# Kernel tuning notes

Measured on AMD Instinct MI355X. Metric: run time of the kernel, lower is better.

Reference implementation:

```python
import jax, jax.numpy as jnp
import numpy as np

B, T, D, H, L, F, V, BANDS = 16, 512, 1024, 8, 6, 4096, 30000, 16
RES = [1, 1, 2, 2, 4, 4, 8, 8]  # per-head K/V resolution schedule
HD = D // H


def setup_inputs() -> dict:
    key = jax.random.key(0)
    ks = iter(jax.random.split(key, 64))
    s = 0.02
    p = {
        "tokens": jax.random.randint(next(ks), (B, T), 0, V, dtype=jnp.int32),
        "embed": jax.random.normal(next(ks), (V, D), jnp.float32) * s,
        "pos_embed": jax.random.normal(next(ks), (T, D), jnp.float32) * s,
        "Wq": jax.random.normal(next(ks), (L, D, D), jnp.float32) * s,
        "bq": jnp.zeros((L, D), jnp.float32),
        "Wk": jax.random.normal(next(ks), (L, D, D), jnp.float32) * s,
        "bk": jnp.zeros((L, D), jnp.float32),
        "Wv": jax.random.normal(next(ks), (L, D, D), jnp.float32) * s,
        "bv": jnp.zeros((L, D), jnp.float32),
        "Wo": jax.random.normal(next(ks), (L, D, D), jnp.float32) * s,
        "bo": jnp.zeros((L, D), jnp.float32),
        "ln1_g": jnp.ones((L, D), jnp.float32),
        "ln1_b": jnp.zeros((L, D), jnp.float32),
        "ln2_g": jnp.ones((L, D), jnp.float32),
        "ln2_b": jnp.zeros((L, D), jnp.float32),
        "W1": jax.random.normal(next(ks), (L, D, F), jnp.float32) * s,
        "b1": jnp.zeros((L, F), jnp.float32),
        "W2": jax.random.normal(next(ks), (L, F, D), jnp.float32) * s,
        "b2": jnp.zeros((L, D), jnp.float32),
        "gates": jnp.ones((L, H, BANDS), jnp.float32),
        "lnf_g": jnp.ones((D,), jnp.float32),
        "lnf_b": jnp.zeros((D,), jnp.float32),
    }
    return p


def _ln(x, g, b, eps=1e-5):
    mu = jnp.mean(x, -1, keepdims=True)
    var = jnp.var(x, -1, keepdims=True)
    return (x - mu) * jax.lax.rsqrt(var + eps) * g + b


def _hfa_attention(x, Wq, bq, Wk, bk, Wv, bv, Wo, bo, gates_l):
    # x: [B,T,D]; per-head resolution schedule + spectral band gating.
    q = (x @ Wq + bq).reshape(B, T, H, HD).transpose(0, 2, 1, 3)  # [B,H,T,HD]
    k = (x @ Wk + bk).reshape(B, T, H, HD).transpose(0, 2, 1, 3)
    v = (x @ Wv + bv).reshape(B, T, H, HD).transpose(0, 2, 1, 3)
    nb = T // 2 + 1
    band_of_bin = (jnp.arange(nb) * BANDS) // nb  # map rfft bin -> spectral band
    scale = 1.0 / np.sqrt(HD)
    outs = []
    for h in range(H):
        r = RES[h]
        kh = k[:, h].reshape(B, T // r, r, HD).mean(2)  # pooled keys [B,T/r,HD]
        vh = v[:, h].reshape(B, T // r, r, HD).mean(2)
        scores = jnp.einsum("btd,bsd->bts", q[:, h], kh) * scale
        attn = jax.nn.softmax(scores, axis=-1)
        o = jnp.einsum("bts,bsd->btd", attn, vh)  # [B,T,HD]
        # spectral band gating along sequence axis
        g = gates_l[h][band_of_bin]  # [nb]
        f = jnp.fft.rfft(o, axis=1) * g[None, :, None]
        o = jnp.fft.irfft(f, n=T, axis=1)
        outs.append(o)
    out = jnp.concatenate(outs, axis=-1)  # [B,T,D]
    return out @ Wo + bo


def reference(tokens, embed, pos_embed, Wq, bq, Wk, bk, Wv, bv, Wo, bo,
              ln1_g, ln1_b, ln2_g, ln2_b, W1, b1, W2, b2, gates, lnf_g, lnf_b):
    x = embed[tokens] + pos_embed[jnp.arange(T)][None, :, :]  # [B,T,D]
    for l in range(L):
        h = _ln(x, ln1_g[l], ln1_b[l])
        x = x + _hfa_attention(h, Wq[l], bq[l], Wk[l], bk[l], Wv[l], bv[l],
                               Wo[l], bo[l], gates[l])
        h = _ln(x, ln2_g[l], ln2_b[l])
        ff = jax.nn.gelu(h @ W1[l] + b1[l], approximate=False) @ W2[l] + b2[l]
        x = x + ff
    return _ln(x, lnf_g, lnf_b)
```

## Files before the change

kernel.cpp:

```cpp
#include <hip/hip_runtime.h>
#include <hip/hip_bf16.h>
#include <math.h>

#define Bn 16
#define Tn 512
#define Dn 1024
#define Hn 8
#define Ln 6
#define Fn 4096
#define HDn 128

typedef __attribute__((ext_vector_type(8))) short short8;
typedef __attribute__((ext_vector_type(4))) float f32x4;

__device__ __forceinline__ float bf2f(unsigned short u){
  union{float f; unsigned int i;} c; c.i = ((unsigned int)u)<<16; return c.f;
}
__device__ __forceinline__ unsigned short f2bf(float f){
  union{float f; unsigned int i;} c; c.f=f;
  unsigned int r = c.i + 0x7fffu + ((c.i>>16)&1u);
  return (unsigned short)(r>>16);
}
__device__ __forceinline__ int pref_of(int h){
  int g = h >> 1;
  return (2048 - (2048 >> g)) + (h & 1) * (512 >> g);
}

#define GLOAD(gp, lp) __builtin_amdgcn_global_load_lds( \
    (const __attribute__((address_space(1))) void*)(const void*)(gp), \
    (__attribute__((address_space(3))) void*)(void*)(lp), 16, 0, 0)

__global__ __launch_bounds__(256) void embed_kernel(
    const int* __restrict__ tok, const float* __restrict__ emb,
    const float* __restrict__ pos, float* __restrict__ x){
  long row = blockIdx.x;
  int t = (int)(row & (Tn-1));
  int tk = tok[row];
  int d = threadIdx.x*4;
  float4 e = *(const float4*)(emb + (long)tk*Dn + d);
  float4 p = *(const float4*)(pos + (long)t*Dn + d);
  float4 r; r.x=e.x+p.x; r.y=e.y+p.y; r.z=e.z+p.z; r.w=e.w+p.w;
  *(float4*)(x + row*(long)Dn + d) = r;
}

template<int OUTBF>
__global__ __launch_bounds__(256) void ln_kernel(
    const float* __restrict__ x, const float* __restrict__ g,
    const float* __restrict__ b, void* __restrict__ outp){
  long row = blockIdx.x;
  const float* xr = x + row*(long)Dn;
  int tid = threadIdx.x;
  float4 v4 = *(const float4*)(xr + tid*4);
  float s  = v4.x+v4.y+v4.z+v4.w;
  float s2 = v4.x*v4.x + v4.y*v4.y + v4.z*v4.z + v4.w*v4.w;
  #pragma unroll
  for (int o=32;o;o>>=1){ s += __shfl_xor(s,o); s2 += __shfl_xor(s2,o); }
  __shared__ float rs[4], rs2[4];
  int w = tid>>6;
  if ((tid&63)==0){ rs[w]=s; rs2[w]=s2; }
  __syncthreads();
  s  = rs[0]+rs[1]+rs[2]+rs[3];
  s2 = rs2[0]+rs2[1]+rs2[2]+rs2[3];
  float mu  = s*(1.f/Dn);
  float var = s2*(1.f/Dn) - mu*mu;
  float rstd = rsqrtf(var + 1e-5f);
  float4 gg = *(const float4*)(g + tid*4);
  float4 bb = *(const float4*)(b + tid*4);
  float o0 = (v4.x-mu)*rstd*gg.x + bb.x;
  float o1 = (v4.y-mu)*rstd*gg.y + bb.y;
  float o2 = (v4.z-mu)*rstd*gg.z + bb.z;
  float o3 = (v4.w-mu)*rstd*gg.w + bb.w;
  if (OUTBF){
    unsigned short* o = (unsigned short*)outp + row*(long)Dn + tid*4;
    o[0]=f2bf(o0); o[1]=f2bf(o1); o[2]=f2bf(o2); o[3]=f2bf(o3);
  } else {
    float* o = (float*)outp + row*(long)Dn + tid*4;
    o[0]=o0; o[1]=o1; o[2]=o2; o[3]=o3;
  }
}

__global__ __launch_bounds__(256) void transpose_w(
    const float* __restrict__ W, unsigned short* __restrict__ WT, int Kd, int Nd){
  __shared__ float tile[32][33];
  long lofs = (long)blockIdx.z * Kd * Nd;
  int n0 = blockIdx.x*32, k0 = blockIdx.y*32;
  int tx = threadIdx.x & 31, ty = threadIdx.x >> 5;
  #pragma unroll
  for (int i=0;i<4;i++){
    int kk = k0 + ty + i*8;
    tile[ty+i*8][tx] = W[lofs + (long)kk*Nd + n0 + tx];
  }
  __syncthreads();
  #pragma unroll
  for (int i=0;i<4;i++){
    int nn = n0 + ty + i*8;
    WT[lofs + (long)nn*Kd + k0 + tx] = f2bf(tile[tx][ty+i*8]);
  }
}

__global__ __launch_bounds__(256) void pack_bias(
    const float* __restrict__ bq, const float* __restrict__ bk,
    const float* __restrict__ bv, float* __restrict__ bqkv){
  int i = blockIdx.x*256 + threadIdx.x;
  int l = i / (3*Dn); int r = i - l*3*Dn; int w = r / Dn; int d = r - w*Dn;
  const float* src = (w==0)? bq : ((w==1)? bk : bv);
  bqkv[i] = src[l*Dn + d];
}

__global__ __launch_bounds__(512) void ckern(
    const float* __restrict__ gates, float* __restrict__ cbuf){
  int lh = blockIdx.x;
  __shared__ float gb[16];
  if (threadIdx.x < 16) gb[threadIdx.x] = gates[lh*16 + threadIdx.x];
  __syncthreads();
  int m = threadIdx.x;
  float acc = gb[0];
  for (int j=1;j<256;j++){
    int band = (j*16)/257;
    int kmod = (j*m) & 511;
    acc += 2.f*gb[band]*cosf(1.2271846303085129e-2f * (float)kmod);
  }
  acc += gb[15] * ((m & 1) ? -1.f : 1.f);
  cbuf[lh*512 + m] = acc * (1.f/512.f);
}

__global__ __launch_bounds__(256) void gfill(
    const float* __restrict__ cbuf, unsigned short* __restrict__ G){
  long idx = (long)blockIdx.x*256 + threadIdx.x;
  int lh = (int)(idx >> 18);
  int rem = (int)(idx & 262143);
  int t = rem >> 9, s = rem & 511;
  G[idx] = f2bf(cbuf[lh*512 + ((t - s) & 511)]);
}

__global__ __launch_bounds__(256) void pool_kernel(
    const unsigned short* __restrict__ kin, const unsigned short* __restrict__ vin,
    unsigned short* __restrict__ kp, unsigned short* __restrict__ vTp){
  long idx = (long)blockIdx.x*256 + threadIdx.x;
  if (idx >= (long)Bn*1920*HDn) return;
  long rem = idx; int hh = 0; int S = 512;
  for (hh=0; hh<8; hh++){
    S = 512 >> (hh>>1);
    long seg = (long)Bn*S*HDn;
    if (rem < seg) break;
    rem -= seg;
  }
  int r = 512 / S;
  int d = (int)(rem % HDn);
  long t2 = rem / HDn;
  int s = (int)(t2 % S);
  int b = (int)(t2 / S);
  const unsigned short* kb = kin + ((long)(b*Tn + s*r))*Dn + hh*HDn + d;
  const unsigned short* vb = vin + ((long)(b*Tn + s*r))*Dn + hh*HDn + d;
  float ks=0.f, vs=0.f;
  for (int j=0;j<r;j++){ ks += bf2f(kb[(long)j*Dn]); vs += bf2f(vb[(long)j*Dn]); }
  float inv = 1.f/(float)r;
  int pref=0;
  for (int g2=0; g2<hh; g2++) pref += 512 >> (g2>>1);
  long segb = (long)Bn*HDn*pref;
  kp [segb + ((long)b*S + s)*HDn + d] = f2bf(ks*inv);
  vTp[segb + ((long)b*HDn + d)*S + s] = f2bf(vs*inv);
}

__global__ __launch_bounds__(256) void softmax_all(
    const float* __restrict__ sc, unsigned short* __restrict__ at){
  long rid = (long)blockIdx.x*4 + (threadIdx.x >> 6);
  int head = (int)(rid >> 13);
  int rih  = (int)(rid & 8191);
  int g = head >> 1;
  int S = 512 >> g;
  int NV = S >> 6;
  long base = (long)Bn*Tn*pref_of(head) + (long)rih*S;
  const float* r = sc + base;
  int lane = threadIdx.x & 63;
  float vals[8];
  float mx = -1e30f;
  #pragma unroll
  for (int i=0;i<8;i++){
    if (i < NV){ vals[i] = r[lane + i*64] * 0.08838834764831845f; mx = fmaxf(mx, vals[i]); }
  }
  #pragma unroll
  for (int o=32;o;o>>=1) mx = fmaxf(mx, __shfl_xor(mx, o));
  float sum = 0.f;
  #pragma unroll
  for (int i=0;i<8;i++){
    if (i < NV){ vals[i] = expf(vals[i]-mx); sum += vals[i]; }
  }
  #pragma unroll
  for (int o=32;o;o>>=1) sum += __shfl_xor(sum, o);
  float inv = 1.f/sum;
  unsigned short* ab = at + base;
  #pragma unroll
  for (int i=0;i<8;i++){
    if (i < NV) ab[lane + i*64] = f2bf(vals[i]*inv);
  }
}

template<int MODE>
__global__ __launch_bounds__(256)
void gemm_kernel(const unsigned short* __restrict__ A, int lda, long sAb, long sAh,
                 const unsigned short* __restrict__ Bt, int ldb, long sBb, long sBh,
                 void* __restrict__ Cout, int ldc, long sCb, long sCh,
                 const float* __restrict__ bias, long sbias,
                 int zshift, int zmask,
                 int M, int N, int K)
{
  __shared__ unsigned short AB[2][2][128*64];
  int z = blockIdx.z;
  int zb = z & zmask, zh = z >> zshift;
  const unsigned short* Az = A + (long)zb*sAb + (long)zh*sAh;
  const unsigned short* Bz = Bt + (long)zb*sBb + (long)zh*sBh;
  const float* biasz = bias ? (bias + (long)zh*sbias) : nullptr;
  int m0 = blockIdx.y*128, n0 = blockIdx.x*128;
  int tid = threadIdx.x;
  int lane = tid & 63, wid = tid >> 6;
  int wm = wid >> 1, wn = wid & 1;
  f32x4 zero4 = {0.f,0.f,0.f,0.f};
  f32x4 acc[4][4];
  #pragma unroll
  for (int m=0;m<4;m++)
    #pragma unroll
    for (int n=0;n<4;n++)
      acc[m][n] = zero4;
  const int r16 = lane & 15, kq = lane >> 4;

  auto stage = [&](int buf, int k0){
    #pragma unroll
    for (int i=0;i<4;i++){
      int chunk = i*256 + tid;
      int row = chunk >> 3, c = chunk & 7;
      int cg = (c ^ (row & 7)) * 8;
      int gm = m0 + row; gm = gm < M ? gm : M-1;
      GLOAD(Az + (long)gm*lda + k0 + cg, AB[buf][0] + (i*256 + wid*64)*8);
    }
    #pragma unroll
    for (int i=0;i<4;i++){
      int chunk = i*256 + tid;
      int row = chunk >> 3, c = chunk & 7;
      int cg = (c ^ (row & 7)) * 8;
      int gn = n0 + row; gn = gn < N ? gn : N-1;
      GLOAD(Bz + (long)gn*ldb + k0 + cg, AB[buf][1] + (i*256 + wid*64)*8);
    }
  };

  int NT = K >> 6;
  stage(0, 0);
  for (int t = 0; t < NT; t++){
    if (t + 1 < NT){
      stage((t+1)&1, (t+1)*64);
      asm volatile("s_waitcnt vmcnt(8)" ::: "memory");
    } else {
      asm volatile("s_waitcnt vmcnt(0)" ::: "memory");
    }
    __builtin_amdgcn_s_barrier();
    const unsigned short* As = AB[t&1][0];
    const unsigned short* Bs = AB[t&1][1];
    #pragma unroll
    for (int kk=0; kk<64; kk+=32){
      short8 af[4], bfr[4];
      int kb = (kk + kq*8) * 2;
      #pragma unroll
      for (int m=0;m<4;m++){
        int row = wm*64 + m*16 + r16;
        af[m] = *(const short8*)((const char*)As + row*128 + (kb ^ ((row & 7) << 4)));
      }
      #pragma unroll
      for (int n=0;n<4;n++){
        int row = wn*64 + n*16 + r16;
        bfr[n] = *(const short8*)((const char*)Bs + row*128 + (kb ^ ((row & 7) << 4)));
      }
      #pragma unroll
      for (int m=0;m<4;m++)
        #pragma unroll
        for (int n=0;n<4;n++)
          acc[m][n] = __builtin_amdgcn_mfma_f32_16x16x32_bf16(af[m], bfr[n], acc[m][n], 0, 0, 0);
    }
    __builtin_amdgcn_s_barrier();
  }
  #pragma unroll
  for (int n=0;n<4;n++){
    int col = n0 + wn*64 + n*16 + r16;
    if (col >= N) continue;
    float bvv = 0.f;
    if (MODE != 0 && biasz != nullptr) bvv = biasz[col];
    #pragma unroll
    for (int m=0;m<4;m++){
      #pragma unroll
      for (int e=0;e<4;e++){
        int row = m0 + wm*64 + m*16 + kq*4 + e;
        if (row >= M) continue;
        float vv = acc[m][n][e] + bvv;
        long cidx = (long)zb*sCb + (long)zh*sCh + (long)row*ldc + col;
        if (MODE == 0)      ((float*)Cout)[cidx] = vv;
        else                ((unsigned short*)Cout)[cidx] = f2bf(vv);
      }
    }
  }
}

__global__ __launch_bounds__(256)
void scores_all(const unsigned short* __restrict__ q,
                const unsigned short* __restrict__ kp,
                float* __restrict__ sc)
{
  __shared__ unsigned short AB[2][2][128*64];
  int z = blockIdx.z;
  int zb = z & 15, zh = z >> 4;
  int g = zh >> 1;
  int S = 512 >> g;
  int n0 = blockIdx.x*128;
  if (n0 >= S) return;
  int pf = pref_of(zh);
  const unsigned short* Az = q  + (long)zb*Tn*Dn + (long)zh*HDn;
  const unsigned short* Bz = kp + (long)Bn*HDn*pf + (long)zb*S*HDn;
  float* Cz = sc + (long)Bn*Tn*pf + (long)zb*Tn*S;
  int m0 = blockIdx.y*128;
  int tid = threadIdx.x;
  int lane = tid & 63, wid = tid >> 6;
  int wm = wid >> 1, wn = wid & 1;
  f32x4 zero4 = {0.f,0.f,0.f,0.f};
  f32x4 acc[4][4];
  #pragma unroll
  for (int m=0;m<4;m++)
    #pragma unroll
    for (int n=0;n<4;n++)
      acc[m][n] = zero4;
  const int r16 = lane & 15, kq = lane >> 4;

  auto stage = [&](int buf, int k0){
    #pragma unroll
    for (int i=0;i<4;i++){
      int chunk = i*256 + tid;
      int row = chunk >> 3, c = chunk & 7;
      int cg = (c ^ (row & 7)) * 8;
      GLOAD(Az + (long)(m0 + row)*Dn + k0 + cg, AB[buf][0] + (i*256 + wid*64)*8);
    }
    #pragma unroll
    for (int i=0;i<4;i++){
      int chunk = i*256 + tid;
      int row = chunk >> 3, c = chunk & 7;
      int cg = (c ^ (row & 7)) * 8;
      int gn = n0 + row; gn = gn < S ? gn : S-1;
      GLOAD(Bz + (long)gn*HDn + k0 + cg, AB[buf][1] + (i*256 + wid*64)*8);
    }
  };

  stage(0, 0);
  stage(1, 64);
  #pragma unroll
  for (int t = 0; t < 2; t++){
    if (t == 0) { asm volatile("s_waitcnt vmcnt(8)" ::: "memory"); }
    else        { asm volatile("s_waitcnt vmcnt(0)" ::: "memory"); }
    __builtin_amdgcn_s_barrier();
    const unsigned short* As = AB[t][0];
    const unsigned short* Bs = AB[t][1];
    #pragma unroll
    for (int kk=0; kk<64; kk+=32){
      short8 af[4], bfr[4];
      int kb = (kk + kq*8) * 2;
      #pragma unroll
      for (int m=0;m<4;m++){
        int row = wm*64 + m*16 + r16;
        af[m] = *(const short8*)((const char*)As + row*128 + (kb ^ ((row & 7) << 4)));
      }
      #pragma unroll
      for (int n=0;n<4;n++){
        int row = wn*64 + n*16 + r16;
        bfr[n] = *(const short8*)((const char*)Bs + row*128 + (kb ^ ((row & 7) << 4)));
      }
      #pragma unroll
      for (int m=0;m<4;m++)
        #pragma unroll
        for (int n=0;n<4;n++)
          acc[m][n] = __builtin_amdgcn_mfma_f32_16x16x32_bf16(af[m], bfr[n], acc[m][n], 0, 0, 0);
    }
    __builtin_amdgcn_s_barrier();
  }
  #pragma unroll
  for (int n=0;n<4;n++){
    int col = n0 + wn*64 + n*16 + r16;
    if (col >= S) continue;
    #pragma unroll
    for (int m=0;m<4;m++){
      #pragma unroll
      for (int e=0;e<4;e++){
        int row = m0 + wm*64 + m*16 + kq*4 + e;
        Cz[(long)row*S + col] = acc[m][n][e];
      }
    }
  }
}

__global__ __launch_bounds__(256)
void pv_all(const unsigned short* __restrict__ vTp,
            const unsigned short* __restrict__ at,
            unsigned short* __restrict__ oT)
{
  __shared__ unsigned short AB[2][2][128*64];
  int z = blockIdx.z;
  int zb = z & 15, zh = z >> 4;
  int g = zh >> 1;
  int S = 512 >> g;
  int pf = pref_of(zh);
  const unsigned short* Az = vTp + (long)Bn*HDn*pf + (long)zb*HDn*S;
  const unsigned short* Bz = at  + (long)Bn*Tn*pf  + (long)zb*Tn*S;
  unsigned short* Cz = oT + (long)zh*Bn*HDn*Tn + (long)zb*HDn*Tn;
  int n0 = blockIdx.x*128;
  int tid = threadIdx.x;
  int lane = tid & 63, wid = tid >> 6;
  int wm = wid >> 1, wn = wid & 1;
  f32x4 zero4 = {0.f,0.f,0.f,0.f};
  f32x4 acc[4][4];
  #pragma unroll
  for (int m=0;m<4;m++)
    #pragma unroll
    for (int n=0;n<4;n++)
      acc[m][n] = zero4;
  const int r16 = lane & 15, kq = lane >> 4;

  auto stage = [&](int buf, int k0){
    #pragma unroll
    for (int i=0;i<4;i++){
      int chunk = i*256 + tid;
      int row = chunk >> 3, c = chunk & 7;
      int cg = (c ^ (row & 7)) * 8;
      GLOAD(Az + (long)row*S + k0 + cg, AB[buf][0] + (i*256 + wid*64)*8);
    }
    #pragma unroll
    for (int i=0;i<4;i++){
      int chunk = i*256 + tid;
      int row = chunk >> 3, c = chunk & 7;
      int cg = (c ^ (row & 7)) * 8;
      GLOAD(Bz + (long)(n0 + row)*S + k0 + cg, AB[buf][1] + (i*256 + wid*64)*8);
    }
  };

  int NT = S >> 6;
  stage(0, 0);
  for (int t = 0; t < NT; t++){
    if (t + 1 < NT){
      stage((t+1)&1, (t+1)*64);
      asm volatile("s_waitcnt vmcnt(8)" ::: "memory");
    } else {
      asm volatile("s_waitcnt vmcnt(0)" ::: "memory");
    }
    __builtin_amdgcn_s_barrier();
    const unsigned short* As = AB[t&1][0];
    const unsigned short* Bs = AB[t&1][1];
    #pragma unroll
    for (int kk=0; kk<64; kk+=32){
      short8 af[4], bfr[4];
      int kb = (kk + kq*8) * 2;
      #pragma unroll
      for (int m=0;m<4;m++){
        int row = wm*64 + m*16 + r16;
        af[m] = *(const short8*)((const char*)As + row*128 + (kb ^ ((row & 7) << 4)));
      }
      #pragma unroll
      for (int n=0;n<4;n++){
        int row = wn*64 + n*16 + r16;
        bfr[n] = *(const short8*)((const char*)Bs + row*128 + (kb ^ ((row & 7) << 4)));
      }
      #pragma unroll
      for (int m=0;m<4;m++)
        #pragma unroll
        for (int n=0;n<4;n++)
          acc[m][n] = __builtin_amdgcn_mfma_f32_16x16x32_bf16(af[m], bfr[n], acc[m][n], 0, 0, 0);
    }
    __builtin_amdgcn_s_barrier();
  }
  #pragma unroll
  for (int n=0;n<4;n++){
    int col = n0 + wn*64 + n*16 + r16;
    #pragma unroll
    for (int m=0;m<4;m++){
      #pragma unroll
      for (int e=0;e<4;e++){
        int row = wm*64 + m*16 + kq*4 + e;
        Cz[(long)row*Tn + col] = f2bf(acc[m][n][e]);
      }
    }
  }
}

template<int MODE, int Mt, int Nt, int Kt, long SBH, long SCH, int BIASST>
__global__ __launch_bounds__(256)
void gemm_big(const unsigned short* __restrict__ A,
              const unsigned short* __restrict__ Bt,
              void* __restrict__ Cout,
              const float* __restrict__ bias)
{
  __shared__ char shraw[2][32768];
  int zh = blockIdx.z;
  const unsigned short* Bz = Bt + (long)zh*SBH;
  const float* biasz = bias + (long)zh*BIASST;
  int m0 = blockIdx.y*128, n0 = blockIdx.x*128;
  int tid = threadIdx.x;
  int lane = tid & 63, wid = tid >> 6;
  int wm = wid >> 1, wn = wid & 1;
  f32x4 zero4 = {0.f,0.f,0.f,0.f};
  f32x4 acc[4][4];
  #pragma unroll
  for (int m=0;m<4;m++)
    #pragma unroll
    for (int n=0;n<4;n++)
      acc[m][n] = zero4;
  const int r16 = lane & 15, kq = lane >> 4;

  const unsigned short* pA[4];
  const unsigned short* pB[4];
  #pragma unroll
  for (int i=0;i<4;i++){
    int chunk = i*256 + tid;
    int row = chunk >> 3, c = chunk & 7;
    int cg = (c ^ (row & 7)) * 8;
    pA[i] = A  + (long)(m0 + row)*Kt + cg;
    pB[i] = Bz + (long)(n0 + row)*Kt + cg;
  }
  auto stage = [&](int buf, int k0){
    unsigned short* As = (unsigned short*)shraw[buf];
    #pragma unroll
    for (int i=0;i<4;i++) GLOAD(pA[i] + k0, As + (i*256 + wid*64)*8);
    #pragma unroll
    for (int i=0;i<4;i++) GLOAD(pB[i] + k0, As + 8192 + (i*256 + wid*64)*8);
  };

  constexpr int NT = Kt/64;
  stage(0, 0);
  for (int t = 0; t < NT; t++){
    if (t + 1 < NT){
      stage((t+1)&1, (t+1)*64);
      asm volatile("s_waitcnt vmcnt(8)" ::: "memory");
    } else {
      asm volatile("s_waitcnt vmcnt(0)" ::: "memory");
    }
    __builtin_amdgcn_s_barrier();
    const unsigned short* As = (const unsigned short*)shraw[t&1];
    const unsigned short* Bs = As + 8192;
    #pragma unroll
    for (int kk=0; kk<64; kk+=32){
      short8 af[4], bfr[4];
      int kb = (kk + kq*8) * 2;
      #pragma unroll
      for (int m=0;m<4;m++){
        int row = wm*64 + m*16 + r16;
        af[m] = *(const short8*)((const char*)As + row*128 + (kb ^ ((row & 7) << 4)));
      }
      #pragma unroll
      for (int n=0;n<4;n++){
        int row = wn*64 + n*16 + r16;
        bfr[n] = *(const short8*)((const char*)Bs + row*128 + (kb ^ ((row & 7) << 4)));
      }
      #pragma unroll
      for (int m=0;m<4;m++)
        #pragma unroll
        for (int n=0;n<4;n++)
          acc[m][n] = __builtin_amdgcn_mfma_f32_16x16x32_bf16(af[m], bfr[n], acc[m][n], 0, 0, 0);
    }
    __builtin_amdgcn_s_barrier();
  }

  if (MODE == 1 || MODE == 2){
    unsigned short* shb = (unsigned short*)&shraw[0][0];
    #pragma unroll
    for (int n=0;n<4;n++){
      int col = wn*64 + n*16 + r16;
      float bvv = biasz[n0 + col];
      #pragma unroll
      for (int m=0;m<4;m++){
        #pragma unroll
        for (int e=0;e<4;e++){
          int row = wm*64 + m*16 + kq*4 + e;
          float vv = acc[m][n][e] + bvv;
          if (MODE == 2) vv = 0.5f*vv*(1.f + erff(vv*0.7071067811865475f));
          shb[row*136 + col] = f2bf(vv);
        }
      }
    }
    __syncthreads();
    #pragma unroll
    for (int i=0;i<8;i++){
      int chunk = i*256 + tid;
      int row = chunk >> 4, col = (chunk & 15)*8;
      short8 vv8 = *(const short8*)(shb + row*136 + col);
      *(short8*)((unsigned short*)Cout + (long)zh*SCH +
                 (long)(m0 + row)*Nt + n0 + col) = vv8;
    }
  } else {
    float* shf = (float*)&shraw[0][0];
    #pragma unroll
    for (int ph=0; ph<2; ph++){
      __syncthreads();
      if (wm == ph){
        #pragma unroll
        for (int n=0;n<4;n++){
          int col = wn*64 + n*16 + r16;
          float bvv = biasz[n0 + col];
          #pragma unroll
          for (int m=0;m<4;m++){
            #pragma unroll
            for (int e=0;e<4;e++){
              int rl = m*16 + kq*4 + e;
              shf[rl*136 + col] = acc[m][n][e] + bvv;
            }
          }
        }
      }
      __syncthreads();
      #pragma unroll
      for (int i=0;i<8;i++){
        int chunk = i*256 + tid;
        int row = chunk >> 5, col = (chunk & 31)*4;
        float4 vv = *(const float4*)(shf + row*136 + col);
        float* cp = (float*)Cout + (long)(m0 + ph*64 + row)*Nt + n0 + col;
        float4 o = *(const float4*)cp;
        o.x += vv.x; o.y += vv.y; o.z += vv.z; o.w += vv.w;
        *(float4*)cp = o;
      }
    }
  }
}

extern "C" void kernel_launch(void* const* d_in, const int* in_sizes, int n_in,
                              void* d_out, int out_size, void* d_ws, size_t ws_size,
                              hipStream_t stream){
  const int*   tokens = (const int*)  d_in[0];
  const float* embedp = (const float*)d_in[1];
  const float* pos    = (const float*)d_in[2];
  const float* Wq  = (const float*)d_in[3];
  const float* bq  = (const float*)d_in[4];
  const float* Wk  = (const float*)d_in[5];
  const float* bk  = (const float*)d_in[6];
  const float* Wv  = (const float*)d_in[7];
  const float* bv  = (const float*)d_in[8];
  const float* Wo  = (const float*)d_in[9];
  const float* bo  = (const float*)d_in[10];
  const float* ln1g= (const float*)d_in[11];
  const float* ln1b= (const float*)d_in[12];
  const float* ln2g= (const float*)d_in[13];
  const float* ln2b= (const float*)d_in[14];
  const float* W1  = (const float*)d_in[15];
  const float* b1  = (const float*)d_in[16];
  const float* W2  = (const float*)d_in[17];
  const float* b2  = (const float*)d_in[18];
  const float* gates=(const float*)d_in[19];
  const float* lnfg= (const float*)d_in[20];
  const float* lnfb= (const float*)d_in[21];
  float* out = (float*)d_out;

  char* base = (char*)d_ws;
  size_t off = 0;
  auto take = [&](size_t bytes)->char*{
    char* p = base + off;
    off = (off + bytes + 255) & ~(size_t)255;
    return p;
  };
  unsigned short* WqT = (unsigned short*)take((size_t)Ln*Dn*Dn*2);
  unsigned short* WkT = (unsigned short*)take((size_t)Ln*Dn*Dn*2);
  unsigned short* WvT = (unsigned short*)take((size_t)Ln*Dn*Dn*2);
  unsigned short* WoT = (unsigned short*)take((size_t)Ln*Dn*Dn*2);
  unsigned short* W1T = (unsigned short*)take((size_t)Ln*Dn*Fn*2);
  unsigned short* W2T = (unsigned short*)take((size_t)Ln*Dn*Fn*2);
  unsigned short* G   = (unsigned short*)take((size_t)Ln*Hn*Tn*Tn*2);
  float*          cbuf= (float*)take((size_t)Ln*Hn*Tn*4);
  float*          bqkv= (float*)take((size_t)Ln*3*Dn*4);
  float*          x   = (float*)take((size_t)Bn*Tn*Dn*4);
  unsigned short* hbuf= (unsigned short*)take((size_t)Bn*Tn*Dn*2);
  unsigned short* q   = (unsigned short*)take((size_t)Bn*Tn*Dn*2);
  unsigned short* k   = (unsigned short*)take((size_t)Bn*Tn*Dn*2);
  unsigned short* v   = (unsigned short*)take((size_t)Bn*Tn*Dn*2);
  unsigned short* kp  = (unsigned short*)take((size_t)Bn*1920*HDn*2);
  unsigned short* vTp = (unsigned short*)take((size_t)Bn*1920*HDn*2);
  unsigned short* ao  = (unsigned short*)take((size_t)Bn*Tn*Dn*2);
  unsigned short* ff1 = (unsigned short*)take((size_t)Bn*Tn*Fn*2);
  unsigned short* attnA = (unsigned short*)take((size_t)Bn*1920*Tn*2);
  if (off > ws_size) return;
  float* scoresA = (float*)ff1;
  unsigned short* oT = k;

  transpose_w<<<dim3(Dn/32, Dn/32, Ln), 256, 0, stream>>>(Wq, WqT, Dn, Dn);
  transpose_w<<<dim3(Dn/32, Dn/32, Ln), 256, 0, stream>>>(Wk, WkT, Dn, Dn);
  transpose_w<<<dim3(Dn/32, Dn/32, Ln), 256, 0, stream>>>(Wv, WvT, Dn, Dn);
  transpose_w<<<dim3(Dn/32, Dn/32, Ln), 256, 0, stream>>>(Wo, WoT, Dn, Dn);
  transpose_w<<<dim3(Fn/32, Dn/32, Ln), 256, 0, stream>>>(W1, W1T, Dn, Fn);
  transpose_w<<<dim3(Dn/32, Fn/32, Ln), 256, 0, stream>>>(W2, W2T, Fn, Dn);
  pack_bias<<<(Ln*3*Dn)/256, 256, 0, stream>>>(bq, bk, bv, bqkv);
  ckern<<<Ln*Hn, 512, 0, stream>>>(gates, cbuf);
  gfill<<<(Ln*Hn*Tn*Tn)/256, 256, 0, stream>>>(cbuf, G);
  embed_kernel<<<Bn*Tn, 256, 0, stream>>>(tokens, embedp, pos, x);

  const int MT = Bn*Tn;

  for (int l=0; l<Ln; l++){
    ln_kernel<1><<<MT, 256, 0, stream>>>(x, ln1g + l*Dn, ln1b + l*Dn, hbuf);
    gemm_big<1, 8192, Dn, Dn, (long)Ln*Dn*Dn, (long)Bn*Tn*Dn, Dn>
        <<<dim3(Dn/128, MT/128, 3), 256, 0, stream>>>(
        hbuf, WqT + (size_t)l*Dn*Dn, q, bqkv + (size_t)l*3*Dn);
    pool_kernel<<<((long)Bn*1920*HDn + 255)/256, 256, 0, stream>>>(k, v, kp, vTp);

    scores_all<<<dim3(4, Tn/128, 128), 256, 0, stream>>>(q, kp, scoresA);
    softmax_all<<<(8*MT)/4, 256, 0, stream>>>(scoresA, attnA);
    pv_all<<<dim3(Tn/128, 1, 128), 256, 0, stream>>>(vTp, attnA, oT);

    gemm_kernel<1><<<dim3(1, Tn/128, 128), 256, 0, stream>>>(
        G + (size_t)(l*Hn)*Tn*Tn, Tn, 0L, (long)Tn*Tn,
        oT, Tn, (long)HDn*Tn, (long)Bn*HDn*Tn,
        ao, Dn, (long)Tn*Dn, (long)HDn,
        nullptr, 0L, 4, 15,
        Tn, HDn, Tn);
    gemm_big<3, 8192, Dn, Dn, 0L, 0L, 0>
        <<<dim3(Dn/128, MT/128, 1), 256, 0, stream>>>(
        ao, WoT + (size_t)l*Dn*Dn, x, bo + l*Dn);
    ln_kernel<1><<<MT, 256, 0, stream>>>(x, ln2g + l*Dn, ln2b + l*Dn, hbuf);
    gemm_big<2, 8192, Fn, Dn, 0L, 0L, 0>
        <<<dim3(Fn/128, MT/128, 1), 256, 0, stream>>>(
        hbuf, W1T + (size_t)l*Dn*Fn, ff1, b1 + l*Fn);
    gemm_big<3, 8192, Dn, Fn, 0L, 0L, 0>
        <<<dim3(Dn/128, MT/128, 1), 256, 0, stream>>>(
        ff1, W2T + (size_t)l*Dn*Fn, x, b2 + l*Dn);
  }
  ln_kernel<0><<<MT, 256, 0, stream>>>(x, lnfg, lnfb, out);
}
```

Before: 2.877 ms.

## Pool LN output before K/V projection to shrink K/V GEMM work

Pooling and linear projection commute, so the normalized activations are mean-pooled per resolution group first and the K/V projections run only on the pooled rows, grouped per head pair. Packed K/V weights and biases are built once at setup, and a small transpose kernel produces the V-transposed layout. This removes the full-resolution K and V GEMMs for the coarser heads and the separate pool pass over K/V. The main GEMM's pipeline is also reordered to wait after compute and to raise wave priority around the MFMA block, which may reduce load/compute overlap.

Measured after the change: 2.777 ms. -3.5%, faster.

```diff
diff --git a/kernel.cpp b/kernel.cpp
--- a/kernel.cpp
+++ b/kernel.cpp
@@ -11,6 +11,7 @@
 #define HDn 128
 
 typedef __attribute__((ext_vector_type(8))) short short8;
+typedef __attribute__((ext_vector_type(4))) short short4v;
 typedef __attribute__((ext_vector_type(4))) float f32x4;
 
 __device__ __forceinline__ float bf2f(unsigned short u){
@@ -24,6 +25,9 @@
 __device__ __forceinline__ int pref_of(int h){
   int g = h >> 1;
   return (2048 - (2048 >> g)) + (h & 1) * (512 >> g);
+}
+__device__ __forceinline__ int kvoff_of(int g){
+  return (g==0)?0:(g==1)?8192:(g==2)?12288:14336;
 }
 
 #define GLOAD(gp, lp) __builtin_amdgcn_global_load_lds( \
@@ -98,13 +102,28 @@
   }
 }
 
-__global__ __launch_bounds__(256) void pack_bias(
-    const float* __restrict__ bq, const float* __restrict__ bk,
-    const float* __restrict__ bv, float* __restrict__ bqkv){
+__global__ __launch_bounds__(256) void pack_wkv(
+    const unsigned short* __restrict__ WkT, const unsigned short* __restrict__ WvT,
+    unsigned short* __restrict__ wkvT){
+  int i8 = blockIdx.x*256 + threadIdx.x;
+  int c8 = i8 & 127;
+  int r  = (i8 >> 7) & 511;
+  int g  = (i8 >> 16) & 3;
+  int l  = i8 >> 18;
+  const unsigned short* src = (r < 256)
+      ? WkT + ((long)l<<20) + (long)(g*256 + r)*1024 + c8*8
+      : WvT + ((long)l<<20) + (long)(g*256 + (r-256))*1024 + c8*8;
+  *(short8*)(wkvT + (long)i8*8) = *(const short8*)src;
+}
+
+__global__ __launch_bounds__(256) void pack_bkv(
+    const float* __restrict__ bk, const float* __restrict__ bv,
+    float* __restrict__ bkv){
   int i = blockIdx.x*256 + threadIdx.x;
-  int l = i / (3*Dn); int r = i - l*3*Dn; int w = r / Dn; int d = r - w*Dn;
-  const float* src = (w==0)? bq : ((w==1)? bk : bv);
-  bqkv[i] = src[l*Dn + d];
+  int c = i & 511;
+  int g = (i >> 9) & 3;
+  int l = i >> 11;
+  bkv[i] = (c < 256) ? bk[l*1024 + g*256 + c] : bv[l*1024 + g*256 + (c-256)];
 }
 
 __global__ __launch_bounds__(512) void ckern(
@@ -133,33 +152,52 @@
   G[idx] = f2bf(cbuf[lh*512 + ((t - s) & 511)]);
 }
 
-__global__ __launch_bounds__(256) void pool_kernel(
-    const unsigned short* __restrict__ kin, const unsigned short* __restrict__ vin,
-    unsigned short* __restrict__ kp, unsigned short* __restrict__ vTp){
-  long idx = (long)blockIdx.x*256 + threadIdx.x;
-  if (idx >= (long)Bn*1920*HDn) return;
-  long rem = idx; int hh = 0; int S = 512;
-  for (hh=0; hh<8; hh++){
-    S = 512 >> (hh>>1);
-    long seg = (long)Bn*S*HDn;
-    if (rem < seg) break;
-    rem -= seg;
-  }
-  int r = 512 / S;
-  int d = (int)(rem % HDn);
-  long t2 = rem / HDn;
-  int s = (int)(t2 % S);
-  int b = (int)(t2 / S);
-  const unsigned short* kb = kin + ((long)(b*Tn + s*r))*Dn + hh*HDn + d;
-  const unsigned short* vb = vin + ((long)(b*Tn + s*r))*Dn + hh*HDn + d;
-  float ks=0.f, vs=0.f;
-  for (int j=0;j<r;j++){ ks += bf2f(kb[(long)j*Dn]); vs += bf2f(vb[(long)j*Dn]); }
+__global__ __launch_bounds__(256) void pool_x(
+    const unsigned short* __restrict__ hbuf, unsigned short* __restrict__ P){
+  int rid = blockIdx.x;
+  int g, S, idx;
+  if (rid < 4096){ g=1; S=256; idx=rid; }
+  else if (rid < 6144){ g=2; S=128; idx=rid-4096; }
+  else { g=3; S=64; idx=rid-6144; }
+  int r = 1 << g;
+  int b = idx / S, s = idx - b*S;
+  const unsigned short* src = hbuf + ((long)(b*512 + s*r))*1024 + threadIdx.x*4;
+  float a0=0.f, a1=0.f, a2=0.f, a3=0.f;
+  for (int j=0;j<r;j++){
+    short4v v = *(const short4v*)(src + (long)j*1024);
+    a0 += bf2f((unsigned short)v[0]); a1 += bf2f((unsigned short)v[1]);
+    a2 += bf2f((unsigned short)v[2]); a3 += bf2f((unsigned short)v[3]);
+  }
   float inv = 1.f/(float)r;
-  int pref=0;
-  for (int g2=0; g2<hh; g2++) pref += 512 >> (g2>>1);
-  long segb = (long)Bn*HDn*pref;
-  kp [segb + ((long)b*S + s)*HDn + d] = f2bf(ks*inv);
-  vTp[segb + ((long)b*HDn + d)*S + s] = f2bf(vs*inv);
+  unsigned short* dst = P + (long)rid*1024 + threadIdx.x*4;
+  dst[0]=f2bf(a0*inv); dst[1]=f2bf(a1*inv); dst[2]=f2bf(a2*inv); dst[3]=f2bf(a3*inv);
+}
+
+__global__ __launch_bounds__(256) void vtrans(
+    const unsigned short* __restrict__ kvbuf, unsigned short* __restrict__ vTp){
+  __shared__ unsigned short tile[32][33];
+  int z = blockIdx.z;
+  int h = z >> 4, b = z & 15;
+  int g = h >> 1, dlt = h & 1;
+  int S = 512 >> g;
+  int s0 = blockIdx.x*32;
+  if (s0 >= S) return;
+  int d0 = blockIdx.y*32;
+  int kvbase = kvoff_of(g) + b*S;
+  int colbase = 256 + dlt*128 + d0;
+  int tx = threadIdx.x & 31, ty = threadIdx.x >> 5;
+  #pragma unroll
+  for (int i=0;i<4;i++){
+    int s = s0 + ty + i*8;
+    tile[ty+i*8][tx] = kvbuf[(long)(kvbase + s)*512 + colbase + tx];
+  }
+  __syncthreads();
+  long basep = (long)Bn*HDn*pref_of(h);
+  #pragma unroll
+  for (int i=0;i<4;i++){
+    int d = d0 + ty + i*8;
+    vTp[basep + ((long)(b*128 + d))*S + s0 + tx] = tile[tx][ty+i*8];
+  }
 }
 
 __global__ __launch_bounds__(256) void softmax_all(
@@ -300,19 +338,19 @@
 
 __global__ __launch_bounds__(256)
 void scores_all(const unsigned short* __restrict__ q,
-                const unsigned short* __restrict__ kp,
+                const unsigned short* __restrict__ kvbuf,
                 float* __restrict__ sc)
 {
   __shared__ unsigned short AB[2][2][128*64];
   int z = blockIdx.z;
   int zb = z & 15, zh = z >> 4;
-  int g = zh >> 1;
+  int g = zh >> 1, dlt = zh & 1;
   int S = 512 >> g;
   int n0 = blockIdx.x*128;
   if (n0 >= S) return;
   int pf = pref_of(zh);
-  const unsigned short* Az = q  + (long)zb*Tn*Dn + (long)zh*HDn;
-  const unsigned short* Bz = kp + (long)Bn*HDn*pf + (long)zb*S*HDn;
+  const unsigned short* Az = q + (long)zb*Tn*Dn + (long)zh*HDn;
+  const unsigned short* Bz = kvbuf + (long)(kvoff_of(g) + zb*S)*512 + dlt*128;
   float* Cz = sc + (long)Bn*Tn*pf + (long)zb*Tn*S;
   int m0 = blockIdx.y*128;
   int tid = threadIdx.x;
@@ -341,7 +379,7 @@
       int row = chunk >> 3, c = chunk & 7;
       int cg = (c ^ (row & 7)) * 8;
       int gn = n0 + row; gn = gn < S ? gn : S-1;
-      GLOAD(Bz + (long)gn*HDn + k0 + cg, AB[buf][1] + (i*256 + wid*64)*8);
+      GLOAD(Bz + (long)gn*512 + k0 + cg, AB[buf][1] + (i*256 + wid*64)*8);
     }
   };
 
@@ -483,6 +521,112 @@
   }
 }
 
+__global__ __launch_bounds__(256)
+void gemm_kv(const unsigned short* __restrict__ hbuf,
+             const unsigned short* __restrict__ P,
+             const unsigned short* __restrict__ wkvT_l,
+             unsigned short* __restrict__ kvbuf,
+             const float* __restrict__ bkv_l)
+{
+  __shared__ char shraw[2][32768];
+  int zh = blockIdx.z;
+  int Mg = 8192 >> zh;
+  int m0 = blockIdx.y*128;
+  if (m0 >= Mg) return;
+  int n0 = blockIdx.x*128;
+  const unsigned short* Az = (zh==0) ? hbuf
+      : P + (long)((zh==1)?0:(zh==2)?4096:6144)*1024;
+  const unsigned short* Bz = wkvT_l + (long)zh*512*1024;
+  int kvo = kvoff_of(zh);
+  int tid = threadIdx.x;
+  int lane = tid & 63, wid = tid >> 6;
+  int wm = wid >> 1, wn = wid & 1;
+  f32x4 zero4 = {0.f,0.f,0.f,0.f};
+  f32x4 acc[4][4];
+  #pragma unroll
+  for (int m=0;m<4;m++)
+    #pragma unroll
+    for (int n=0;n<4;n++)
+      acc[m][n] = zero4;
+  const int r16 = lane & 15, kq = lane >> 4;
+
+  auto stage = [&](int buf, int k0){
+    unsigned short* As = (unsigned short*)shraw[buf];
+    #pragma unroll
+    for (int i=0;i<4;i++){
+      int chunk = i*256 + tid;
+      int row = chunk >> 3, c = chunk & 7;
+      int cg = (c ^ (row & 7)) * 8;
+      GLOAD(Az + (long)(m0 + row)*1024 + k0 + cg, As + (i*256 + wid*64)*8);
+    }
+    #pragma unroll
+    for (int i=0;i<4;i++){
+      int chunk = i*256 + tid;
+      int row = chunk >> 3, c = chunk & 7;
+      int cg = (c ^ (row & 7)) * 8;
+      GLOAD(Bz + (long)(n0 + row)*1024 + k0 + cg, As + 8192 + (i*256 + wid*64)*8);
+    }
+  };
+
+  const int NT = 16;
+  stage(0, 0);
+  for (int t = 0; t < NT; t++){
+    if (t + 1 < NT){
+      stage((t+1)&1, (t+1)*64);
+      asm volatile("s_waitcnt vmcnt(8)" ::: "memory");
+    } else {
+      asm volatile("s_waitcnt vmcnt(0)" ::: "memory");
+    }
+    __builtin_amdgcn_s_barrier();
+    const unsigned short* As = (const unsigned short*)shraw[t&1];
+    const unsigned short* Bs = As + 8192;
+    #pragma unroll
+    for (int kk=0; kk<64; kk+=32){
+      short8 af[4], bfr[4];
+      int kb = (kk + kq*8) * 2;
+      #pragma unroll
+      for (int m=0;m<4;m++){
+        int row = wm*64 + m*16 + r16;
+        af[m] = *(const short8*)((const char*)As + row*128 + (kb ^ ((row & 7) << 4)));
+      }
+      #pragma unroll
+      for (int n=0;n<4;n++){
+        int row = wn*64 + n*16 + r16;
+        bfr[n] = *(const short8*)((const char*)Bs + row*128 + (kb ^ ((row & 7) << 4)));
+      }
+      #pragma unroll
+      for (int m=0;m<4;m++)
+        #pragma unroll
+        for (int n=0;n<4;n++)
+          acc[m][n] = __builtin_amdgcn_mfma_f32_16x16x32_bf16(af[m], bfr[n], acc[m][n], 0, 0, 0);
+    }
+    __builtin_amdgcn_s_barrier();
+  }
+
+  unsigned short* shb = (unsigned short*)&shraw[0][0];
+  #pragma unroll
+  for (int n=0;n<4;n++){
+    int col = wn*64 + n*16 + r16;
+    float bvv = bkv_l[zh*512 + n0 + col];
+    #pragma unroll
+    for (int m=0;m<4;m++){
+      #pragma unroll
+      for (int e=0;e<4;e++){
+        int row = wm*64 + m*16 + kq*4 + e;
+        shb[row*136 + col] = f2bf(acc[m][n][e] + bvv);
+      }
+    }
+  }
+  __syncthreads();
+  #pragma unroll
+  for (int i=0;i<8;i++){
+    int chunk = i*256 + tid;
+    int row = chunk >> 4, col = (chunk & 15)*8;
+    short8 vv8 = *(const short8*)(shb + row*136 + col);
+    *(short8*)(kvbuf + (long)(kvo + m0 + row)*512 + n0 + col) = vv8;
+  }
+}
+
 template<int MODE, int Mt, int Nt, int Kt, long SBH, long SCH, int BIASST>
 __global__ __launch_bounds__(256)
 void gemm_big(const unsigned short* __restrict__ A,
@@ -527,14 +671,10 @@
 
   constexpr int NT = Kt/64;
   stage(0, 0);
+  asm volatile("s_waitcnt vmcnt(0)" ::: "memory");
+  __builtin_amdgcn_s_barrier();
   for (int t = 0; t < NT; t++){
-    if (t + 1 < NT){
-      stage((t+1)&1, (t+1)*64);
-      asm volatile("s_waitcnt vmcnt(8)" ::: "memory");
-    } else {
-      asm volatile("s_waitcnt vmcnt(0)" ::: "memory");
-    }
-    __builtin_amdgcn_s_barrier();
+    if (t + 1 < NT) stage((t+1)&1, (t+1)*64);
     const unsigned short* As = (const unsigned short*)shraw[t&1];
     const unsigned short* Bs = As + 8192;
     #pragma unroll
@@ -551,12 +691,15 @@
         int row = wn*64 + n*16 + r16;
         bfr[n] = *(const short8*)((const char*)Bs + row*128 + (kb ^ ((row & 7) << 4)));
       }
+      __builtin_amdgcn_s_setprio(1);
       #pragma unroll
       for (int m=0;m<4;m++)
         #pragma unroll
         for (int n=0;n<4;n++)
           acc[m][n] = __builtin_amdgcn_mfma_f32_16x16x32_bf16(af[m], bfr[n], acc[m][n], 0, 0, 0);
-    }
+      __builtin_amdgcn_s_setprio(0);
+    }
+    if (t + 1 < NT) asm volatile("s_waitcnt vmcnt(0)" ::: "memory");
     __builtin_amdgcn_s_barrier();
   }
 
@@ -661,22 +804,22 @@
   unsigned short* WoT = (unsigned short*)take((size_t)Ln*Dn*Dn*2);
   unsigned short* W1T = (unsigned short*)take((size_t)Ln*Dn*Fn*2);
   unsigned short* W2T = (unsigned short*)take((size_t)Ln*Dn*Fn*2);
+  unsigned short* wkvT= (unsigned short*)take((size_t)Ln*4*512*1024*2);
+  float*          bkv = (float*)take((size_t)Ln*4*512*4);
   unsigned short* G   = (unsigned short*)take((size_t)Ln*Hn*Tn*Tn*2);
   float*          cbuf= (float*)take((size_t)Ln*Hn*Tn*4);
-  float*          bqkv= (float*)take((size_t)Ln*3*Dn*4);
   float*          x   = (float*)take((size_t)Bn*Tn*Dn*4);
   unsigned short* hbuf= (unsigned short*)take((size_t)Bn*Tn*Dn*2);
   unsigned short* q   = (unsigned short*)take((size_t)Bn*Tn*Dn*2);
-  unsigned short* k   = (unsigned short*)take((size_t)Bn*Tn*Dn*2);
-  unsigned short* v   = (unsigned short*)take((size_t)Bn*Tn*Dn*2);
-  unsigned short* kp  = (unsigned short*)take((size_t)Bn*1920*HDn*2);
+  unsigned short* kvbuf=(unsigned short*)take((size_t)15360*512*2);
+  unsigned short* P   = (unsigned short*)take((size_t)7168*1024*2);
   unsigned short* vTp = (unsigned short*)take((size_t)Bn*1920*HDn*2);
+  unsigned short* oT  = (unsigned short*)take((size_t)Hn*Bn*HDn*Tn*2);
   unsigned short* ao  = (unsigned short*)take((size_t)Bn*Tn*Dn*2);
   unsigned short* ff1 = (unsigned short*)take((size_t)Bn*Tn*Fn*2);
   unsigned short* attnA = (unsigned short*)take((size_t)Bn*1920*Tn*2);
   if (off > ws_size) return;
   float* scoresA = (float*)ff1;
-  unsigned short* oT = k;
 
   transpose_w<<<dim3(Dn/32, Dn/32, Ln), 256, 0, stream>>>(Wq, WqT, Dn, Dn);
   transpose_w<<<dim3(Dn/32, Dn/32, Ln), 256, 0, stream>>>(Wk, WkT, Dn, Dn);
@@ -684,7 +827,8 @@
   transpose_w<<<dim3(Dn/32, Dn/32, Ln), 256, 0, stream>>>(Wo, WoT, Dn, Dn);
   transpose_w<<<dim3(Fn/32, Dn/32, Ln), 256, 0, stream>>>(W1, W1T, Dn, Fn);
   transpose_w<<<dim3(Dn/32, Fn/32, Ln), 256, 0, stream>>>(W2, W2T, Fn, Dn);
-  pack_bias<<<(Ln*3*Dn)/256, 256, 0, stream>>>(bq, bk, bv, bqkv);
+  pack_wkv<<<(Ln*4*512*128)/256, 256, 0, stream>>>(WkT, WvT, wkvT);
+  pack_bkv<<<(Ln*4*512)/256, 256, 0, stream>>>(bk, bv, bkv);
   ckern<<<Ln*Hn, 512, 0, stream>>>(gates, cbuf);
   gfill<<<(Ln*Hn*Tn*Tn)/256, 256, 0, stream>>>(cbuf, G);
   embed_kernel<<<Bn*Tn, 256, 0, stream>>>(tokens, embedp, pos, x);
@@ -693,12 +837,15 @@
 
   for (int l=0; l<Ln; l++){
     ln_kernel<1><<<MT, 256, 0, stream>>>(x, ln1g + l*Dn, ln1b + l*Dn, hbuf);
-    gemm_big<1, 8192, Dn, Dn, (long)Ln*Dn*Dn, (long)Bn*Tn*Dn, Dn>
-        <<<dim3(Dn/128, MT/128, 3), 256, 0, stream>>>(
-        hbuf, WqT + (size_t)l*Dn*Dn, q, bqkv + (size_t)l*3*Dn);
-    pool_kernel<<<((long)Bn*1920*HDn + 255)/256, 256, 0, stream>>>(k, v, kp, vTp);
-
-    scores_all<<<dim3(4, Tn/128, 128), 256, 0, stream>>>(q, kp, scoresA);
+    pool_x<<<7168, 256, 0, stream>>>(hbuf, P);
+    gemm_big<1, 8192, Dn, Dn, 0L, 0L, 0>
+        <<<dim3(Dn/128, MT/128, 1), 256, 0, stream>>>(
+        hbuf, WqT + (size_t)l*Dn*Dn, q, bq + l*Dn);
+    gemm_kv<<<dim3(4, 64, 4), 256, 0, stream>>>(
+        hbuf, P, wkvT + (size_t)l*4*512*1024, kvbuf, bkv + (size_t)l*4*512);
+    vtrans<<<dim3(16, 4, 128), 256, 0, stream>>>(kvbuf, vTp);
+
+    scores_all<<<dim3(4, Tn/128, 128), 256, 0, stream>>>(q, kvbuf, scoresA);
     softmax_all<<<(8*MT)/4, 256, 0, stream>>>(scoresA, attnA);
     pv_all<<<dim3(Tn/128, 1, 128), 256, 0, stream>>>(vTp, attnA, oT);
 
```
